# Kernel tuning notes

Measured on AMD Instinct MI355X. Metric: run time of the kernel, lower is better.

The kernel has to match this reference:

```python
import jax, jax.numpy as jnp
import numpy as np

N, E, D_IN, H, C, N_GRAPHS = 50000, 800000, 128, 2, 64, 50
D_HID = H * C  # 128
NEG_SLOPE = 0.2
EPS = 1e-16


def glorot(key, shape):
    fan_in, fan_out = shape[0], shape[-1]
    lim = jnp.sqrt(6.0 / (fan_in + fan_out))
    return jax.random.uniform(key, shape, jnp.float32, -lim, lim)


def setup_inputs() -> dict:
    key = jax.random.key(0)
    ks = jax.random.split(key, 12)
    x = jax.random.normal(ks[0], (N, D_IN), jnp.float32)
    edge_index = jax.random.randint(ks[1], (2, E), 0, N, jnp.int64)
    batch = jnp.sort(jax.random.randint(ks[2], (N,), 0, N_GRAPHS, jnp.int64))
    # GATConv layer 1: in=128 -> heads=2, out=64
    W1 = glorot(ks[3], (D_IN, H * C))
    as1 = glorot(ks[4], (1, H, C)).reshape(H, C)
    ad1 = glorot(ks[5], (1, H, C)).reshape(H, C)
    b1 = jnp.zeros((H * C,), jnp.float32)
    # GATConv layer 2: in=128 -> heads=2, out=64
    W2 = glorot(ks[6], (D_HID, H * C))
    as2 = glorot(ks[7], (1, H, C)).reshape(H, C)
    ad2 = glorot(ks[8], (1, H, C)).reshape(H, C)
    b2 = jnp.zeros((H * C,), jnp.float32)
    # Linear head: 128 -> 1
    Wh = glorot(ks[9], (D_HID, 1))
    bh = jnp.zeros((1,), jnp.float32)
    return {"x": x, "edge_index": edge_index, "batch": batch,
            "W1": W1, "as1": as1, "ad1": ad1, "b1": b1,
            "W2": W2, "as2": as2, "ad2": ad2, "b2": b2,
            "Wh": Wh, "bh": bh}


def gat_conv(x, src, dst, W, a_src, a_dst, bias):
    # PyG GATConv (concat=True, add_self_loops applied by caller, eval mode)
    n = x.shape[0]
    h = (x @ W).reshape(n, H, C)                       # [N,H,C]
    al_s = jnp.einsum('nhc,hc->nh', h, a_src)          # [N,H]
    al_d = jnp.einsum('nhc,hc->nh', h, a_dst)
    e = jax.nn.leaky_relu(al_s[src] + al_d[dst], NEG_SLOPE)  # [E',H]
    # segment softmax over incoming edges of each dst node
    e_max = jax.ops.segment_max(e, dst, num_segments=n)
    e = jnp.exp(e - e_max[dst])
    denom = jax.ops.segment_sum(e, dst, num_segments=n)
    alpha = e / (denom[dst] + EPS)                     # [E',H]
    out = jax.ops.segment_sum(alpha[:, :, None] * h[src], dst, num_segments=n)
    return out.reshape(n, H * C) + bias


def reference(x, edge_index, batch, W1, as1, ad1, b1, W2, as2, ad2, b2, Wh, bh):
    # add self-loops (PyG GATConv default)
    loops = jnp.arange(N, dtype=edge_index.dtype)
    src = jnp.concatenate([edge_index[0], loops])
    dst = jnp.concatenate([edge_index[1], loops])
    h = gat_conv(x, src, dst, W1, as1, ad1, b1)
    h = jax.nn.relu(h)  # dropout is identity in eval mode
    h = gat_conv(h, src, dst, W2, as2, ad2, b2)
    h = jax.nn.relu(h)
    # global mean pool over graphs
    sums = jax.ops.segment_sum(h, batch, num_segments=N_GRAPHS)
    counts = jax.ops.segment_sum(jnp.ones((N, 1), h.dtype), batch, num_segments=N_GRAPHS)
    pooled = sums / jnp.maximum(counts, 1.0)           # [G, 128]
    return pooled @ Wh + bh                            # [G, 1]
```

## Files before the change

### kernel.cpp

```cpp
#include <hip/hip_runtime.h>
#include <hip/hip_fp16.h>
#include <math.h>

#define HD 128
#define NEG_SLOPE 0.2f
#define EPSV 1e-16f
#define TILE 8192

typedef unsigned short ushort_t;
typedef __attribute__((ext_vector_type(8))) short bf16x8;
typedef __attribute__((ext_vector_type(4))) float f32x4;

__device__ inline void bsplit(float x, ushort_t& hi, ushort_t& lo) {
    unsigned u = __float_as_uint(x);
    unsigned hb = (u + 0x7FFFu + ((u >> 16) & 1u)) >> 16;
    hi = (ushort_t)hb;
    float res = x - __uint_as_float(hb << 16);
    unsigned v = __float_as_uint(res);
    lo = (ushort_t)((v + 0x7FFFu + ((v >> 16) & 1u)) >> 16);
}

__global__ __launch_bounds__(256) void part_hist(const int* __restrict__ dst,
                                                 int* __restrict__ tileHist, int E) {
    __shared__ int hist[256];
    int t = threadIdx.x;
    hist[t] = 0;
    __syncthreads();
    int base = blockIdx.x * TILE;
    int end = base + TILE; if (end > E) end = E;
    for (int i = base + t; i < end; i += 256)
        atomicAdd(&hist[dst[i] >> 8], 1);
    __syncthreads();
    tileHist[blockIdx.x * 256 + t] = hist[t];
}

__global__ __launch_bounds__(256) void part_offsets(int* __restrict__ tileHist,
                                                    int* __restrict__ bucketBase,
                                                    int NT) {
    __shared__ int s[256];
    int b = threadIdx.x;
    int total = 0;
    #pragma unroll 8
    for (int t = 0; t < NT; ++t) total += tileHist[t * 256 + b];
    s[b] = total;
    __syncthreads();
    for (int o = 1; o < 256; o <<= 1) {
        int v = (b >= o) ? s[b - o] : 0;
        __syncthreads();
        s[b] += v;
        __syncthreads();
    }
    int base = (b == 0) ? 0 : s[b - 1];
    bucketBase[b] = base;
    if (b == 255) bucketBase[256] = s[255];
    int run = base;
    #pragma unroll 8
    for (int t = 0; t < NT; ++t) {
        int v = tileHist[t * 256 + b];
        tileHist[t * 256 + b] = run;
        run += v;
    }
}

__global__ __launch_bounds__(256) void part_scatter(const int* __restrict__ src,
                                                    const int* __restrict__ dst,
                                                    const int* __restrict__ tileHist,
                                                    int2* __restrict__ part, int E) {
    __shared__ int cur[256];
    int t = threadIdx.x;
    cur[t] = tileHist[blockIdx.x * 256 + t];
    __syncthreads();
    int base = blockIdx.x * TILE;
    int end = base + TILE; if (end > E) end = E;
    for (int i = base + t; i < end; i += 256) {
        int d = dst[i], s = src[i];
        int p = atomicAdd(&cur[d >> 8], 1);
        part[p] = make_int2(s, d);
    }
}

__global__ __launch_bounds__(256) void fine_counts(const int2* __restrict__ part,
                                                   const int* __restrict__ bucketBase,
                                                   int* __restrict__ cnt, int N) {
    __shared__ int hist[256];
    int t = threadIdx.x;
    hist[t] = 0;
    __syncthreads();
    int b = blockIdx.x;
    int s0 = bucketBase[b], s1 = bucketBase[b + 1];
    for (int i = s0 + t; i < s1; i += 256)
        atomicAdd(&hist[part[i].y & 255], 1);
    __syncthreads();
    int d = b * 256 + t;
    if (d < N) cnt[d] = hist[t] + 1;
}

__global__ __launch_bounds__(256) void block_sums(const int* __restrict__ cnt,
                                                  int* __restrict__ bsum, int N) {
    __shared__ int s[4];
    int t = threadIdx.x;
    int i = blockIdx.x * 256 + t;
    int v = (i < N) ? cnt[i] : 0;
    for (int o = 32; o >= 1; o >>= 1) v += __shfl_xor(v, o, 64);
    if ((t & 63) == 0) s[t >> 6] = v;
    __syncthreads();
    if (t == 0) bsum[blockIdx.x] = s[0] + s[1] + s[2] + s[3];
}

__global__ __launch_bounds__(256) void scan_bsums(int* __restrict__ bsum, int NB) {
    __shared__ int s[256];
    __shared__ int carry;
    int t = threadIdx.x;
    if (t == 0) carry = 0;
    __syncthreads();
    for (int base = 0; base < NB; base += 256) {
        int i = base + t;
        int v = (i < NB) ? bsum[i] : 0;
        s[t] = v;
        __syncthreads();
        for (int o = 1; o < 256; o <<= 1) {
            int u = (t >= o) ? s[t - o] : 0;
            __syncthreads();
            s[t] += u;
            __syncthreads();
        }
        int excl = ((t == 0) ? 0 : s[t - 1]) + carry;
        if (i < NB) bsum[i] = excl;
        __syncthreads();
        if (t == 0) carry += s[255];
        __syncthreads();
    }
}

__global__ __launch_bounds__(256) void scatter_scan(const int* __restrict__ cnt,
                                                    const int* __restrict__ bsum,
                                                    int* __restrict__ indptr, int N) {
    __shared__ int s[256];
    int t = threadIdx.x;
    int i = blockIdx.x * 256 + t;
    int v = (i < N) ? cnt[i] : 0;
    s[t] = v;
    __syncthreads();
    for (int o = 1; o < 256; o <<= 1) {
        int u = (t >= o) ? s[t - o] : 0;
        __syncthreads();
        s[t] += u;
        __syncthreads();
    }
    int excl = ((t == 0) ? 0 : s[t - 1]) + bsum[blockIdx.x];
    if (i < N) indptr[i] = excl;
    if (i == N - 1) indptr[N] = excl + v;
}

__global__ __launch_bounds__(256) void csr_scatter(const int2* __restrict__ part,
                                                   const int* __restrict__ bucketBase,
                                                   const int* __restrict__ indptr,
                                                   int* __restrict__ csr, int N) {
    __shared__ int cur[256];
    int t = threadIdx.x;
    int b = blockIdx.x;
    int d = b * 256 + t;
    cur[t] = (d < N) ? indptr[d] : 0;
    __syncthreads();
    int s0 = bucketBase[b], s1 = bucketBase[b + 1];
    for (int i = s0 + t; i < s1; i += 256) {
        int2 e = part[i];
        int p = atomicAdd(&cur[e.y & 255], 1);
        csr[p] = e.x;
    }
    __syncthreads();
    if (d < N) csr[cur[t]] = d;
}

__global__ __launch_bounds__(256) void split_w(const float* __restrict__ W,
                                               ushort_t* __restrict__ Whs,
                                               ushort_t* __restrict__ Wls) {
    int idx = blockIdx.x * 256 + threadIdx.x;
    int j    = idx & 7;
    int lane = (idx >> 3) & 63;
    int ks   = (idx >> 9) & 3;
    int ct   = idx >> 11;
    int n = ct * 16 + (lane & 15);
    int k = ks * 32 + (lane >> 4) * 8 + j;
    ushort_t hi, lo;
    bsplit(W[k * 128 + n], hi, lo);
    Whs[idx] = hi;
    Wls[idx] = lo;
}

__global__ __launch_bounds__(256) void gemm_mfma(const float* __restrict__ A,
                                                 const ushort_t* __restrict__ Whs,
                                                 const ushort_t* __restrict__ Wls,
                                                 const float* __restrict__ a_s,
                                                 const float* __restrict__ a_d,
                                                 __half* __restrict__ h16,
                                                 float* __restrict__ als,
                                                 float* __restrict__ ald, int N) {
    const int gw   = (blockIdx.x * 256 + threadIdx.x) >> 6;
    const int lane = threadIdx.x & 63;
    const int r0   = gw * 32;
    if (r0 >= N) return;
    const int m = lane & 15;
    const int q = lane >> 4;

    bf16x8 ah[2][4], al[2][4];
    #pragma unroll
    for (int t = 0; t < 2; ++t) {
        int row = r0 + t * 16 + m;
        if (row >= N) row = N - 1;
        const float* ap = A + (size_t)row * HD;
        #pragma unroll
        for (int ks = 0; ks < 4; ++ks) {
            float4 v0 = *(const float4*)(ap + ks * 32 + q * 8);
            float4 v1 = *(const float4*)(ap + ks * 32 + q * 8 + 4);
            float vv[8] = {v0.x, v0.y, v0.z, v0.w, v1.x, v1.y, v1.z, v1.w};
            #pragma unroll
            for (int j = 0; j < 8; ++j) {
                ushort_t hb, lb;
                bsplit(vv[j], hb, lb);
                ah[t][ks][j] = (short)hb;
                al[t][ks][j] = (short)lb;
            }
        }
    }

    float ps[2][4] = {{0,0,0,0},{0,0,0,0}};
    float pd[2][4] = {{0,0,0,0},{0,0,0,0}};

    #pragma unroll 1
    for (int ct = 0; ct < 8; ++ct) {
        f32x4 acc0 = {0.f, 0.f, 0.f, 0.f};
        f32x4 acc1 = {0.f, 0.f, 0.f, 0.f};
        #pragma unroll
        for (int ks = 0; ks < 4; ++ks) {
            bf16x8 wh = *(const bf16x8*)(Whs + ((size_t)(ct * 4 + ks) * 64 + lane) * 8);
            bf16x8 wl = *(const bf16x8*)(Wls + ((size_t)(ct * 4 + ks) * 64 + lane) * 8);
            acc0 = __builtin_amdgcn_mfma_f32_16x16x32_bf16(ah[0][ks], wh, acc0, 0, 0, 0);
            acc1 = __builtin_amdgcn_mfma_f32_16x16x32_bf16(ah[1][ks], wh, acc1, 0, 0, 0);
            acc0 = __builtin_amdgcn_mfma_f32_16x16x32_bf16(al[0][ks], wh, acc0, 0, 0, 0);
            acc1 = __builtin_amdgcn_mfma_f32_16x16x32_bf16(al[1][ks], wh, acc1, 0, 0, 0);
            acc0 = __builtin_amdgcn_mfma_f32_16x16x32_bf16(ah[0][ks], wl, acc0, 0, 0, 0);
            acc1 = __builtin_amdgcn_mfma_f32_16x16x32_bf16(ah[1][ks], wl, acc1, 0, 0, 0);
        }
        const int col = ct * 16 + m;
        const float asv = a_s[col], adv = a_d[col];
        #pragma unroll
        for (int reg = 0; reg < 4; ++reg) {
            ps[0][reg] += acc0[reg] * asv;  pd[0][reg] += acc0[reg] * adv;
            ps[1][reg] += acc1[reg] * asv;  pd[1][reg] += acc1[reg] * adv;
            int row0 = r0 + q * 4 + reg;
            if (row0 < N) h16[(size_t)row0 * HD + col] = __float2half(acc0[reg]);
            int row1 = row0 + 16;
            if (row1 < N) h16[(size_t)row1 * HD + col] = __float2half(acc1[reg]);
        }
        if (ct == 3 || ct == 7) {
            int head = ct >> 2;
            #pragma unroll
            for (int t = 0; t < 2; ++t) {
                #pragma unroll
                for (int reg = 0; reg < 4; ++reg) {
                    float vs = ps[t][reg], vd = pd[t][reg];
                    for (int o = 8; o >= 1; o >>= 1) {
                        vs += __shfl_xor(vs, o, 64);
                        vd += __shfl_xor(vd, o, 64);
                    }
                    if (m == 0) {
                        int row = r0 + t * 16 + q * 4 + reg;
                        if (row < N) { als[2 * row + head] = vs; ald[2 * row + head] = vd; }
                    }
                    ps[t][reg] = 0.f;  pd[t][reg] = 0.f;
                }
            }
        }
    }
}

__global__ __launch_bounds__(256) void gat_aggregate(const __half* __restrict__ h,
                                                     const float* __restrict__ als,
                                                     const float* __restrict__ ald,
                                                     const int* __restrict__ indptr,
                                                     const int* __restrict__ csr,
                                                     const float* __restrict__ bias,
                                                     float* __restrict__ out,
                                                     const float* __restrict__ Wh,
                                                     float* __restrict__ svec, int N) {
    int w    = (blockIdx.x * blockDim.x + threadIdx.x) >> 6;
    int lane = threadIdx.x & 63;
    if (w >= N) return;
    int start = indptr[w], end = indptr[w + 1];
    float ad0 = ald[2 * w], ad1 = ald[2 * w + 1];
    const bool head0 = (lane < 32);
    const int cbase = lane * 2;

    float accx = 0.f, accy = 0.f, d0 = 0.f, d1 = 0.f;
    for (int base = start; base < end; base += 64) {
        int i = base + lane;
        float w0 = 0.f, w1 = 0.f; int s = 0;
        if (i < end) {
            s = csr[i];
            float2 av = *(const float2*)&als[2 * s];
            float e0 = av.x + ad0;
            float e1 = av.y + ad1;
            e0 = e0 > 0.f ? e0 : NEG_SLOPE * e0;
            e1 = e1 > 0.f ? e1 : NEG_SLOPE * e1;
            w0 = __expf(e0);
            w1 = __expf(e1);
        }
        d0 += w0; d1 += w1;
        int nl = end - base; if (nl > 64) nl = 64;
        int j = 0;
        for (; j + 8 <= nl; j += 8) {
            int sj[8]; float wa[8];
            #pragma unroll
            for (int u = 0; u < 8; ++u) {
                sj[u] = __shfl(s, j + u, 64);
                float a = __shfl(w0, j + u, 64);
                float b = __shfl(w1, j + u, 64);
                wa[u] = head0 ? a : b;
            }
            __half2 hv[8];
            #pragma unroll
            for (int u = 0; u < 8; ++u)
                hv[u] = *(const __half2*)&h[(size_t)sj[u] * HD + cbase];
            #pragma unroll
            for (int u = 0; u < 8; ++u) {
                float2 f = __half22float2(hv[u]);
                accx += wa[u] * f.x;
                accy += wa[u] * f.y;
            }
        }
        for (; j < nl; ++j) {
            int sjv = __shfl(s, j, 64);
            float a = __shfl(w0, j, 64);
            float b = __shfl(w1, j, 64);
            float wj = head0 ? a : b;
            float2 f = __half22float2(*(const __half2*)&h[(size_t)sjv * HD + cbase]);
            accx += wj * f.x;
            accy += wj * f.y;
        }
    }
    for (int o = 32; o >= 1; o >>= 1) {
        d0 += __shfl_xor(d0, o, 64);
        d1 += __shfl_xor(d1, o, 64);
    }
    float D = (head0 ? d0 : d1) + EPSV;
    float ox = accx / D + bias[cbase];
    float oy = accy / D + bias[cbase + 1];
    ox = ox > 0.f ? ox : 0.f;
    oy = oy > 0.f ? oy : 0.f;

    if (svec) {
        float2 wv = *(const float2*)&Wh[cbase];
        float part = ox * wv.x + oy * wv.y;
        for (int o = 32; o >= 1; o >>= 1) part += __shfl_xor(part, o, 64);
        if (lane == 0) svec[w] = part;
    } else {
        *(float2*)&out[(size_t)w * HD + cbase] = make_float2(ox, oy);
    }
}

__global__ void graph_bounds(const int* __restrict__ batch, int* __restrict__ gstart,
                             int N, int G) {
    int g = blockIdx.x * blockDim.x + threadIdx.x;
    if (g > G) return;
    int lo = 0, hi = N;
    while (lo < hi) {
        int mid = (lo + hi) >> 1;
        if (batch[mid] < g) lo = mid + 1; else hi = mid;
    }
    gstart[g] = lo;
}

__global__ __launch_bounds__(256) void pool_reduce(const float* __restrict__ s,
                                                   const int* __restrict__ gstart,
                                                   const float* __restrict__ bh,
                                                   float* __restrict__ out, int G) {
    __shared__ float partial[4];
    int g = blockIdx.x, t = threadIdx.x;
    int a = gstart[g], b = gstart[g + 1];
    float sum = 0.f;
    for (int i = a + t; i < b; i += 256) sum += s[i];
    for (int o = 32; o >= 1; o >>= 1) sum += __shfl_xor(sum, o, 64);
    if ((t & 63) == 0) partial[t >> 6] = sum;
    __syncthreads();
    if (t == 0) {
        float cnt = (float)(b - a); if (cnt < 1.f) cnt = 1.f;
        out[g] = (partial[0] + partial[1] + partial[2] + partial[3]) / cnt + bh[0];
    }
}

extern "C" void kernel_launch(void* const* d_in, const int* in_sizes, int n_in,
                              void* d_out, int out_size, void* d_ws, size_t ws_size,
                              hipStream_t stream) {
    const float* x     = (const float*)d_in[0];
    const int*   ei    = (const int*)d_in[1];
    const int*   batch = (const int*)d_in[2];
    const float* W1  = (const float*)d_in[3];
    const float* as1 = (const float*)d_in[4];
    const float* ad1 = (const float*)d_in[5];
    const float* b1  = (const float*)d_in[6];
    const float* W2  = (const float*)d_in[7];
    const float* as2 = (const float*)d_in[8];
    const float* ad2 = (const float*)d_in[9];
    const float* b2  = (const float*)d_in[10];
    const float* Wh  = (const float*)d_in[11];
    const float* bh  = (const float*)d_in[12];
    float* out = (float*)d_out;

    const int N = in_sizes[0] / HD;
    const int E = in_sizes[1] / 2;
    const int G = out_size;
    const int* srcp = ei;
    const int* dstp = ei + E;
    const int NB  = (N + 255) / 256;
    const int NBK = (N + 255) / 256;
    const int NT  = (E + TILE - 1) / TILE;

    char* ws = (char*)d_ws;
    size_t off = 0;
    auto alloc = [&](size_t bytes) -> void* {
        void* p = ws + off;
        off += (bytes + 255) & ~(size_t)255;
        return p;
    };
    __half* h16   = (__half*)alloc((size_t)N * HD * 2);
    float* ob     = (float*)alloc((size_t)N * HD * 4);
    float* als    = (float*)alloc((size_t)N * 2 * 4);
    float* ald    = (float*)alloc((size_t)N * 2 * 4);
    float* svec   = (float*)alloc((size_t)N * 4);
    int*   indptr = (int*)  alloc((size_t)(N + 1) * 4);
    int*   cnt    = (int*)  alloc((size_t)N * 4);
    int*   bsum   = (int*)  alloc((size_t)NB * 4);
    int*   csr    = (int*)  alloc((size_t)(E + N) * 4);
    int*   gstart = (int*)  alloc((size_t)(G + 1) * 4);
    int*   tileHist   = (int*)alloc((size_t)NT * 256 * 4);
    int*   bucketBase = (int*)alloc(257 * 4);
    int2*  part   = (int2*) alloc((size_t)E * 8);
    ushort_t* Whs1 = (ushort_t*)alloc(16384 * 2);
    ushort_t* Wls1 = (ushort_t*)alloc(16384 * 2);
    ushort_t* Whs2 = (ushort_t*)alloc(16384 * 2);
    ushort_t* Wls2 = (ushort_t*)alloc(16384 * 2);

    part_hist<<<NT, 256, 0, stream>>>(dstp, tileHist, E);
    part_offsets<<<1, 256, 0, stream>>>(tileHist, bucketBase, NT);
    part_scatter<<<NT, 256, 0, stream>>>(srcp, dstp, tileHist, part, E);
    fine_counts<<<NBK, 256, 0, stream>>>(part, bucketBase, cnt, N);
    block_sums<<<NB, 256, 0, stream>>>(cnt, bsum, N);
    scan_bsums<<<1, 256, 0, stream>>>(bsum, NB);
    scatter_scan<<<NB, 256, 0, stream>>>(cnt, bsum, indptr, N);
    csr_scatter<<<NBK, 256, 0, stream>>>(part, bucketBase, indptr, csr, N);
    graph_bounds<<<1, 64, 0, stream>>>(batch, gstart, N, G);

    split_w<<<64, 256, 0, stream>>>(W1, Whs1, Wls1);
    split_w<<<64, 256, 0, stream>>>(W2, Whs2, Wls2);

    const int nwaves  = (N + 31) / 32;
    const int gblocks = (nwaves + 3) / 4;
    int wgrid = (N * 64 + 255) / 256;

    gemm_mfma<<<gblocks, 256, 0, stream>>>(x, Whs1, Wls1, as1, ad1, h16, als, ald, N);
    gat_aggregate<<<wgrid, 256, 0, stream>>>(h16, als, ald, indptr, csr, b1, ob,
                                             nullptr, nullptr, N);
    gemm_mfma<<<gblocks, 256, 0, stream>>>(ob, Whs2, Wls2, as2, ad2, h16, als, ald, N);
    gat_aggregate<<<wgrid, 256, 0, stream>>>(h16, als, ald, indptr, csr, b2, nullptr,
                                             Wh, svec, N);
    pool_reduce<<<G, 256, 0, stream>>>(svec, gstart, bh, out, G);
}
```

Before: 273.0 us.

## Store layer-1 output in fp16, pack attention weights, shrink GEMM wave tile

The intermediate layer-1 output is now stored as fp16 instead of fp32, and the second GEMM reads it through a templated half loader, halving that buffer's write and read traffic. The aggregation kernel packs both heads' exp weights into one 32-bit fp16 pair, so it needs one shuffle per edge instead of two. It also drops the scalar tail loop by padding to groups of 8 with zero weights, clamping the index to a valid edge. The GEMM drops from 32 to 16 rows per wave, giving more waves and fewer registers at the cost of reloading W more often. Rounding the weights and activations to fp16 adds precision loss.

```diff
diff --git a/kernel.cpp b/kernel.cpp
--- a/kernel.cpp
+++ b/kernel.cpp
@@ -188,7 +188,21 @@
     Wls[idx] = lo;
 }
 
-__global__ __launch_bounds__(256) void gemm_mfma(const float* __restrict__ A,
+__device__ inline void load8(const float* p, float* vv) {
+    float4 a = *(const float4*)p;
+    float4 b = *(const float4*)(p + 4);
+    vv[0]=a.x; vv[1]=a.y; vv[2]=a.z; vv[3]=a.w;
+    vv[4]=b.x; vv[5]=b.y; vv[6]=b.z; vv[7]=b.w;
+}
+__device__ inline void load8(const __half* p, float* vv) {
+    bf16x8 r = *(const bf16x8*)p;
+    #pragma unroll
+    for (int j = 0; j < 8; ++j)
+        vv[j] = __half2float(__ushort_as_half((ushort_t)r[j]));
+}
+
+template <typename TA>
+__global__ __launch_bounds__(256) void gemm_mfma(const TA* __restrict__ A,
                                                  const ushort_t* __restrict__ Whs,
                                                  const ushort_t* __restrict__ Wls,
                                                  const float* __restrict__ a_s,
@@ -198,78 +212,67 @@
                                                  float* __restrict__ ald, int N) {
     const int gw   = (blockIdx.x * 256 + threadIdx.x) >> 6;
     const int lane = threadIdx.x & 63;
-    const int r0   = gw * 32;
+    const int r0   = gw * 16;
     if (r0 >= N) return;
     const int m = lane & 15;
     const int q = lane >> 4;
 
-    bf16x8 ah[2][4], al[2][4];
-    #pragma unroll
-    for (int t = 0; t < 2; ++t) {
-        int row = r0 + t * 16 + m;
+    bf16x8 ah[4], al[4];
+    {
+        int row = r0 + m;
         if (row >= N) row = N - 1;
-        const float* ap = A + (size_t)row * HD;
+        const TA* ap = A + (size_t)row * HD;
         #pragma unroll
         for (int ks = 0; ks < 4; ++ks) {
-            float4 v0 = *(const float4*)(ap + ks * 32 + q * 8);
-            float4 v1 = *(const float4*)(ap + ks * 32 + q * 8 + 4);
-            float vv[8] = {v0.x, v0.y, v0.z, v0.w, v1.x, v1.y, v1.z, v1.w};
+            float vv[8];
+            load8(ap + ks * 32 + q * 8, vv);
             #pragma unroll
             for (int j = 0; j < 8; ++j) {
                 ushort_t hb, lb;
                 bsplit(vv[j], hb, lb);
-                ah[t][ks][j] = (short)hb;
-                al[t][ks][j] = (short)lb;
+                ah[ks][j] = (short)hb;
+                al[ks][j] = (short)lb;
             }
         }
     }
 
-    float ps[2][4] = {{0,0,0,0},{0,0,0,0}};
-    float pd[2][4] = {{0,0,0,0},{0,0,0,0}};
+    float ps[4] = {0,0,0,0};
+    float pd[4] = {0,0,0,0};
 
     #pragma unroll 1
     for (int ct = 0; ct < 8; ++ct) {
-        f32x4 acc0 = {0.f, 0.f, 0.f, 0.f};
-        f32x4 acc1 = {0.f, 0.f, 0.f, 0.f};
+        f32x4 acc = {0.f, 0.f, 0.f, 0.f};
         #pragma unroll
         for (int ks = 0; ks < 4; ++ks) {
             bf16x8 wh = *(const bf16x8*)(Whs + ((size_t)(ct * 4 + ks) * 64 + lane) * 8);
             bf16x8 wl = *(const bf16x8*)(Wls + ((size_t)(ct * 4 + ks) * 64 + lane) * 8);
-            acc0 = __builtin_amdgcn_mfma_f32_16x16x32_bf16(ah[0][ks], wh, acc0, 0, 0, 0);
-            acc1 = __builtin_amdgcn_mfma_f32_16x16x32_bf16(ah[1][ks], wh, acc1, 0, 0, 0);
-            acc0 = __builtin_amdgcn_mfma_f32_16x16x32_bf16(al[0][ks], wh, acc0, 0, 0, 0);
-            acc1 = __builtin_amdgcn_mfma_f32_16x16x32_bf16(al[1][ks], wh, acc1, 0, 0, 0);
-            acc0 = __builtin_amdgcn_mfma_f32_16x16x32_bf16(ah[0][ks], wl, acc0, 0, 0, 0);
-            acc1 = __builtin_amdgcn_mfma_f32_16x16x32_bf16(ah[1][ks], wl, acc1, 0, 0, 0);
+            acc = __builtin_amdgcn_mfma_f32_16x16x32_bf16(ah[ks], wh, acc, 0, 0, 0);
+            acc = __builtin_amdgcn_mfma_f32_16x16x32_bf16(al[ks], wh, acc, 0, 0, 0);
+            acc = __builtin_amdgcn_mfma_f32_16x16x32_bf16(ah[ks], wl, acc, 0, 0, 0);
         }
         const int col = ct * 16 + m;
         const float asv = a_s[col], adv = a_d[col];
         #pragma unroll
         for (int reg = 0; reg < 4; ++reg) {
-            ps[0][reg] += acc0[reg] * asv;  pd[0][reg] += acc0[reg] * adv;
-            ps[1][reg] += acc1[reg] * asv;  pd[1][reg] += acc1[reg] * adv;
-            int row0 = r0 + q * 4 + reg;
-            if (row0 < N) h16[(size_t)row0 * HD + col] = __float2half(acc0[reg]);
-            int row1 = row0 + 16;
-            if (row1 < N) h16[(size_t)row1 * HD + col] = __float2half(acc1[reg]);
+            ps[reg] += acc[reg] * asv;
+            pd[reg] += acc[reg] * adv;
+            int row = r0 + q * 4 + reg;
+            if (row < N) h16[(size_t)row * HD + col] = __float2half(acc[reg]);
         }
         if (ct == 3 || ct == 7) {
             int head = ct >> 2;
             #pragma unroll
-            for (int t = 0; t < 2; ++t) {
-                #pragma unroll
-                for (int reg = 0; reg < 4; ++reg) {
-                    float vs = ps[t][reg], vd = pd[t][reg];
-                    for (int o = 8; o >= 1; o >>= 1) {
-                        vs += __shfl_xor(vs, o, 64);
-                        vd += __shfl_xor(vd, o, 64);
-                    }
-                    if (m == 0) {
-                        int row = r0 + t * 16 + q * 4 + reg;
-                        if (row < N) { als[2 * row + head] = vs; ald[2 * row + head] = vd; }
-                    }
-                    ps[t][reg] = 0.f;  pd[t][reg] = 0.f;
+            for (int reg = 0; reg < 4; ++reg) {
+                float vs = ps[reg], vd = pd[reg];
+                for (int o = 8; o >= 1; o >>= 1) {
+                    vs += __shfl_xor(vs, o, 64);
+                    vd += __shfl_xor(vd, o, 64);
                 }
+                if (m == 0) {
+                    int row = r0 + q * 4 + reg;
+                    if (row < N) { als[2 * row + head] = vs; ald[2 * row + head] = vd; }
+                }
+                ps[reg] = 0.f;  pd[reg] = 0.f;
             }
         }
     }
@@ -281,7 +284,7 @@
                                                      const int* __restrict__ indptr,
                                                      const int* __restrict__ csr,
                                                      const float* __restrict__ bias,
-                                                     float* __restrict__ out,
+                                                     __half* __restrict__ out,
                                                      const float* __restrict__ Wh,
                                                      float* __restrict__ svec, int N) {
     int w    = (blockIdx.x * blockDim.x + threadIdx.x) >> 6;
@@ -295,28 +298,32 @@
     float accx = 0.f, accy = 0.f, d0 = 0.f, d1 = 0.f;
     for (int base = start; base < end; base += 64) {
         int i = base + lane;
-        float w0 = 0.f, w1 = 0.f; int s = 0;
+        int idx = i < end ? i : end - 1;
+        int s = csr[idx];
+        unsigned wpack = 0u;
         if (i < end) {
-            s = csr[i];
             float2 av = *(const float2*)&als[2 * s];
             float e0 = av.x + ad0;
             float e1 = av.y + ad1;
             e0 = e0 > 0.f ? e0 : NEG_SLOPE * e0;
             e1 = e1 > 0.f ? e1 : NEG_SLOPE * e1;
-            w0 = __expf(e0);
-            w1 = __expf(e1);
-        }
-        d0 += w0; d1 += w1;
+            __half p0 = __float2half(__expf(e0));
+            __half p1 = __float2half(__expf(e1));
+            wpack = ((unsigned)__half_as_ushort(p1) << 16) | __half_as_ushort(p0);
+            d0 += __half2float(p0);
+            d1 += __half2float(p1);
+        }
         int nl = end - base; if (nl > 64) nl = 64;
-        int j = 0;
-        for (; j + 8 <= nl; j += 8) {
+        int nb = (nl + 7) >> 3;
+        for (int b = 0; b < nb; ++b) {
+            int j = b * 8;
             int sj[8]; float wa[8];
             #pragma unroll
             for (int u = 0; u < 8; ++u) {
                 sj[u] = __shfl(s, j + u, 64);
-                float a = __shfl(w0, j + u, 64);
-                float b = __shfl(w1, j + u, 64);
-                wa[u] = head0 ? a : b;
+                unsigned wp = (unsigned)__shfl((int)wpack, j + u, 64);
+                unsigned bits = head0 ? (wp & 0xffffu) : (wp >> 16);
+                wa[u] = __half2float(__ushort_as_half((ushort_t)bits));
             }
             __half2 hv[8];
             #pragma unroll
@@ -329,15 +336,6 @@
                 accy += wa[u] * f.y;
             }
         }
-        for (; j < nl; ++j) {
-            int sjv = __shfl(s, j, 64);
-            float a = __shfl(w0, j, 64);
-            float b = __shfl(w1, j, 64);
-            float wj = head0 ? a : b;
-            float2 f = __half22float2(*(const __half2*)&h[(size_t)sjv * HD + cbase]);
-            accx += wj * f.x;
-            accy += wj * f.y;
-        }
     }
     for (int o = 32; o >= 1; o >>= 1) {
         d0 += __shfl_xor(d0, o, 64);
@@ -355,7 +353,8 @@
         for (int o = 32; o >= 1; o >>= 1) part += __shfl_xor(part, o, 64);
         if (lane == 0) svec[w] = part;
     } else {
-        *(float2*)&out[(size_t)w * HD + cbase] = make_float2(ox, oy);
+        *(__half2*)&out[(size_t)w * HD + cbase] =
+            __halves2half2(__float2half(ox), __float2half(oy));
     }
 }
 
@@ -424,7 +423,7 @@
         return p;
     };
     __half* h16   = (__half*)alloc((size_t)N * HD * 2);
-    float* ob     = (float*)alloc((size_t)N * HD * 4);
+    __half* ob16  = (__half*)alloc((size_t)N * HD * 2);
     float* als    = (float*)alloc((size_t)N * 2 * 4);
     float* ald    = (float*)alloc((size_t)N * 2 * 4);
     float* svec   = (float*)alloc((size_t)N * 4);
@@ -454,14 +453,14 @@
     split_w<<<64, 256, 0, stream>>>(W1, Whs1, Wls1);
     split_w<<<64, 256, 0, stream>>>(W2, Whs2, Wls2);
 
-    const int nwaves  = (N + 31) / 32;
+    const int nwaves  = (N + 15) / 16;
     const int gblocks = (nwaves + 3) / 4;
     int wgrid = (N * 64 + 255) / 256;
 
     gemm_mfma<<<gblocks, 256, 0, stream>>>(x, Whs1, Wls1, as1, ad1, h16, als, ald, N);
-    gat_aggregate<<<wgrid, 256, 0, stream>>>(h16, als, ald, indptr, csr, b1, ob,
+    gat_aggregate<<<wgrid, 256, 0, stream>>>(h16, als, ald, indptr, csr, b1, ob16,
                                              nullptr, nullptr, N);
-    gemm_mfma<<<gblocks, 256, 0, stream>>>(ob, Whs2, Wls2, as2, ad2, h16, als, ald, N);
+    gemm_mfma<<<gblocks, 256, 0, stream>>>(ob16, Whs2, Wls2, as2, ad2, h16, als, ald, N);
     gat_aggregate<<<wgrid, 256, 0, stream>>>(h16, als, ald, indptr, csr, b2, nullptr,
                                              Wh, svec, N);
     pool_reduce<<<G, 256, 0, stream>>>(svec, gstart, bh, out, G);
```

New measurement: 264.0 us. 1.03x faster.
